# Kernel tuning notes

Measured on AMD Instinct MI355X. Metric: run time of the kernel, lower is better.

The kernel has to match this reference:

```python
import jax, jax.numpy as jnp
import numpy as np


def setup_inputs() -> dict:
    key = jax.random.key(0)
    k1, k2, k3 = jax.random.split(key, 3)
    vol_shape = (4, 1, 128, 192, 192)   # [B, C, D, H, W]
    dsc_shape = (4, 1, 8, 12, 12)       # PatchGAN-style discriminator logits
    return {
        "dsc_fake": jax.random.normal(k1, dsc_shape, dtype=jnp.float32),
        "predicts": jax.random.normal(k2, vol_shape, dtype=jnp.float32),
        "y_data": jax.random.normal(k3, vol_shape, dtype=jnp.float32),
        "zeros": jnp.zeros(dsc_shape, dtype=jnp.float32),
    }


def reference(dsc_fake, predicts, y_data, zeros):
    # BCE with logits (stable form), target = zeros
    bce = jnp.mean(
        jnp.maximum(dsc_fake, 0.0) - dsc_fake * zeros
        + jnp.log1p(jnp.exp(-jnp.abs(dsc_fake)))
    )
    # L1 loss between target volume and prediction
    g_loss_l1 = jnp.mean(jnp.abs(y_data - predicts))
    # Finite-difference gradient MSE along D, H, W (axes 2,3,4).
    # Original detaches to numpy, so this term carries no gradient.
    yd = jax.lax.stop_gradient(y_data)
    pr = jax.lax.stop_gradient(predicts)
    g_loss_gd = jnp.float32(0.0)
    for ax in (2, 3, 4):
        gy = jnp.abs(jnp.gradient(yd, axis=ax))   # central diff interior, one-sided edges
        gp = jnp.abs(jnp.gradient(pr, axis=ax))
        g_loss_gd = g_loss_gd + jnp.mean((gy - gp) ** 2)
    return bce + 100.0 * g_loss_l1 + 100.0 * g_loss_gd
```

## Files before the change

### kernel.cpp

```cpp
#include <hip/hip_runtime.h>
#include <math.h>

namespace {
constexpr int BATCH = 4;
constexpr int DDIM  = 128;
constexpr int HDIM  = 192;
constexpr int WDIM  = 192;
constexpr long long NTOT = (long long)BATCH * DDIM * HDIM * WDIM;
constexpr int GW    = WDIM / 4;
constexpr int NDSC  = 4 * 1 * 8 * 12 * 12;
constexpr int TH    = 8;
constexpr int SROWS = TH + 2;
constexpr int SGRP  = SROWS * GW;
constexpr int SFL   = SGRP * 4;
constexpr int BLOCK = 512;
constexpr int NWAVE = BLOCK / 64;
constexpr int NCHUNK = (SGRP + 63) / 64;
constexpr int NCOMP = TH * GW;
constexpr int DC    = 16;
constexpr int GRID  = BATCH * (HDIM / TH) * (DDIM / DC);
}

__device__ __forceinline__ float4 ld4(const float* __restrict__ p, long long g) {
    return *(const float4*)(p + 4LL * g);
}

__device__ __forceinline__ void stage2(const float* __restrict__ y,
                                       const float* __restrict__ p,
                                       long long fbase,
                                       float* ldsY, float* ldsP,
                                       int wave, int lane) {
    const int gbase = (wave == NCHUNK - 1) ? (SGRP - 64) : (wave * 64);
    __builtin_amdgcn_global_load_lds(
        (const __attribute__((address_space(1))) void*)(y + fbase + 4LL * (gbase + lane)),
        (__attribute__((address_space(3))) void*)(ldsY + 4 * gbase), 16, 0, 0);
    __builtin_amdgcn_global_load_lds(
        (const __attribute__((address_space(1))) void*)(p + fbase + 4LL * (gbase + lane)),
        (__attribute__((address_space(3))) void*)(ldsP + 4 * gbase), 16, 0, 0);
}

__global__ __launch_bounds__(BLOCK, 6) void vol_kernel(const float* __restrict__ p,
                                                       const float* __restrict__ y,
                                                       float* __restrict__ part) {
    __shared__ __align__(16) float smem[3][2][SFL];

    int bid = blockIdx.x;
    const int dIdx = bid % (DDIM / DC); bid /= (DDIM / DC);
    const int hIdx = bid % (HDIM / TH); bid /= (HDIM / TH);
    const int b    = bid;
    const int d0   = dIdx * DC;
    const int h0   = hIdx * TH;

    const int tid  = threadIdx.x;
    const int lane = tid & 63;
    const int wave = tid >> 6;
    const bool comp = (tid < NCOMP);

    const int g0 = (h0 == 0) ? 0 : ((h0 == HDIM - TH) ? (HDIM - SROWS) : (h0 - 1));
    const long long planeStride = (long long)HDIM * WDIM;
    const long long volBase = (long long)b * DDIM * planeStride + (long long)g0 * WDIM;

    stage2(y, p, volBase + (long long)d0 * planeStride,
           &smem[0][0][0], &smem[0][1][0], wave, lane);
    stage2(y, p, volBase + (long long)(d0 + 1) * planeStride,
           &smem[1][0][0], &smem[1][1][0], wave, lane);

    const int r  = tid / GW;
    const int gw = tid % GW;
    const int h  = h0 + r;
    const int rowOff = h0 - g0;
    const int sf  = ((r + rowOff) * GW + gw) * 4;
    const int hmF = ((h == 0)        ? 0 : -GW) * 4;
    const int hpF = ((h == HDIM - 1) ? 0 :  GW) * 4;
    const float sh  = (h == 0 || h == HDIM - 1) ? 1.f : 0.5f;
    const float swx = (gw == 0)      ? 1.f : 0.5f;
    const float sww = (gw == GW - 1) ? 1.f : 0.5f;
    const bool needL = (lane == 0)  && (gw > 0);
    const bool needR = (lane == 63) && (gw < GW - 1);

    float4 cm2y, cm1y, cm2p, cm1p;
    if (comp) {
        const int dm = (d0 > 0) ? (d0 - 1) : 0;
        const long long gown = (((long long)b * DDIM + dm) * HDIM + h) * GW + gw;
        cm1y = ld4(y, gown); cm1p = ld4(p, gown);
    }

    float l1 = 0.f, gd = 0.f;

    for (int i = 0; i <= DC; ++i) {
        if (i < DC) asm volatile("s_waitcnt vmcnt(2) lgkmcnt(0)" ::: "memory");
        else        asm volatile("s_waitcnt vmcnt(0) lgkmcnt(0)" ::: "memory");
        asm volatile("s_barrier" ::: "memory");

        if (i + 2 <= DC) {
            int dd = d0 + i + 2; if (dd > DDIM - 1) dd = DDIM - 1;
            const int s = (i + 2) % 3;
            stage2(y, p, volBase + (long long)dd * planeStride,
                   &smem[s][0][0], &smem[s][1][0], wave, lane);
        }

        if (comp) {
            const float* curY = &smem[i % 3][0][0];
            const float* curP = &smem[i % 3][1][0];
            const float4 c0y = *(const float4*)(curY + sf);
            const float4 c0p = *(const float4*)(curP + sf);

            if (i >= 1) {
                const int q = d0 + i - 1;
                const float sd = (q == 0 || q == DDIM - 1) ? 1.f : 0.5f;
                float t0;
                t0 = fabsf((c0y.x - cm2y.x) * sd) - fabsf((c0p.x - cm2p.x) * sd); gd += t0 * t0;
                t0 = fabsf((c0y.y - cm2y.y) * sd) - fabsf((c0p.y - cm2p.y) * sd); gd += t0 * t0;
                t0 = fabsf((c0y.z - cm2y.z) * sd) - fabsf((c0p.z - cm2p.z) * sd); gd += t0 * t0;
                t0 = fabsf((c0y.w - cm2y.w) * sd) - fabsf((c0p.w - cm2p.w) * sd); gd += t0 * t0;
            }

            if (i < DC) {
                l1 += fabsf(c0y.x - c0p.x) + fabsf(c0y.y - c0p.y)
                    + fabsf(c0y.z - c0p.z) + fabsf(c0y.w - c0p.w);

                float Ly = __shfl_up(c0y.w, 1, 64);
                float Lp = __shfl_up(c0p.w, 1, 64);
                float Ry = __shfl_down(c0y.x, 1, 64);
                float Rp = __shfl_down(c0p.x, 1, 64);
                if (needL) { Ly = curY[sf - 1]; Lp = curP[sf - 1]; }
                if (needR) { Ry = curY[sf + 4]; Rp = curP[sf + 4]; }
                Ly = gw ? Ly : c0y.x;             Lp = gw ? Lp : c0p.x;
                Ry = (gw == GW - 1) ? c0y.w : Ry; Rp = (gw == GW - 1) ? c0p.w : Rp;

                float t0, gy, gp;
                gy = (c0y.y - Ly) * swx;    gp = (c0p.y - Lp) * swx;
                t0 = fabsf(gy) - fabsf(gp); gd += t0 * t0;
                gy = (c0y.z - c0y.x) * 0.5f; gp = (c0p.z - c0p.x) * 0.5f;
                t0 = fabsf(gy) - fabsf(gp); gd += t0 * t0;
                gy = (c0y.w - c0y.y) * 0.5f; gp = (c0p.w - c0p.y) * 0.5f;
                t0 = fabsf(gy) - fabsf(gp); gd += t0 * t0;
                gy = (Ry - c0y.z) * sww;    gp = (Rp - c0p.z) * sww;
                t0 = fabsf(gy) - fabsf(gp); gd += t0 * t0;

                const float4 yhm = *(const float4*)(curY + sf + hmF);
                const float4 yhp = *(const float4*)(curY + sf + hpF);
                const float4 phm = *(const float4*)(curP + sf + hmF);
                const float4 php = *(const float4*)(curP + sf + hpF);
                t0 = fabsf((yhp.x - yhm.x) * sh) - fabsf((php.x - phm.x) * sh); gd += t0 * t0;
                t0 = fabsf((yhp.y - yhm.y) * sh) - fabsf((php.y - phm.y) * sh); gd += t0 * t0;
                t0 = fabsf((yhp.z - yhm.z) * sh) - fabsf((php.z - phm.z) * sh); gd += t0 * t0;
                t0 = fabsf((yhp.w - yhm.w) * sh) - fabsf((php.w - phm.w) * sh); gd += t0 * t0;
            }

            cm2y = cm1y; cm1y = c0y;
            cm2p = cm1p; cm1p = c0p;
        }
    }

    __shared__ float red1[NWAVE], red2[NWAVE];
    #pragma unroll
    for (int off = 32; off > 0; off >>= 1) {
        l1 += __shfl_down(l1, off, 64);
        gd += __shfl_down(gd, off, 64);
    }
    if (lane == 0) { red1[wave] = l1; red2[wave] = gd; }
    __syncthreads();
    if (tid == 0) {
        float s1 = 0.f, s2 = 0.f;
        #pragma unroll
        for (int w = 0; w < NWAVE; ++w) { s1 += red1[w]; s2 += red2[w]; }
        part[2 * blockIdx.x]     = s1;
        part[2 * blockIdx.x + 1] = s2;
    }
}

__global__ __launch_bounds__(256) void finalize_kernel(const float* __restrict__ dsc,
                                                       const float* __restrict__ part,
                                                       float* __restrict__ out) {
    float l1 = 0.f, gd = 0.f, s = 0.f;
    for (int i = threadIdx.x; i < GRID; i += 256) {
        l1 += part[2 * i];
        gd += part[2 * i + 1];
    }
    for (int i = threadIdx.x; i < NDSC; i += 256) {
        const float x = dsc[i];
        s += fmaxf(x, 0.f) + log1pf(expf(-fabsf(x)));
    }
    __shared__ float a[4], c[4], e[4];
    #pragma unroll
    for (int off = 32; off > 0; off >>= 1) {
        l1 += __shfl_down(l1, off, 64);
        gd += __shfl_down(gd, off, 64);
        s  += __shfl_down(s,  off, 64);
    }
    if ((threadIdx.x & 63) == 0) {
        const int w = threadIdx.x >> 6;
        a[w] = l1; c[w] = gd; e[w] = s;
    }
    __syncthreads();
    if (threadIdx.x == 0) {
        const float bce = (e[0] + e[1] + e[2] + e[3]) / (float)NDSC;
        const float l1m = (a[0] + a[1] + a[2] + a[3]) / (float)NTOT;
        const float gdm = (c[0] + c[1] + c[2] + c[3]) / (float)NTOT;
        out[0] = bce + 100.f * (l1m + gdm);
    }
}

extern "C" void kernel_launch(void* const* d_in, const int* in_sizes, int n_in,
                              void* d_out, int out_size, void* d_ws, size_t ws_size,
                              hipStream_t stream) {
    const float* dsc_fake = (const float*)d_in[0];
    const float* predicts = (const float*)d_in[1];
    const float* y_data   = (const float*)d_in[2];
    float* part = (float*)d_ws;
    float* out  = (float*)d_out;

    vol_kernel<<<GRID, BLOCK, 0, stream>>>(predicts, y_data, part);
    finalize_kernel<<<1, 256, 0, stream>>>(dsc_fake, part, out);
}
```

Before: 194.2 us.

## Fuse finalize into volume kernel with atomic ticket; enlarge tiles, double-buffer

Removes the separate finalize kernel. Each block now accumulates its partial sums with atomics, and the last block, found through a ticket counter, writes the final loss. The BCE term is spread across blocks. Tiles grow to 16 rows by 32 depth slices with 768-thread blocks, and the staging drops from three LDS buffers to two, using __syncthreads instead of hand-written waitcnt. This cuts launch overhead and halo re-reads but shortens the prefetch depth and lowers the block count, which may hurt latency hiding. It also adds a memset call and float atomic nondeterminism.

```diff
diff --git a/kernel.cpp b/kernel.cpp
--- a/kernel.cpp
+++ b/kernel.cpp
@@ -9,16 +9,16 @@
 constexpr long long NTOT = (long long)BATCH * DDIM * HDIM * WDIM;
 constexpr int GW    = WDIM / 4;
 constexpr int NDSC  = 4 * 1 * 8 * 12 * 12;
-constexpr int TH    = 8;
+constexpr int TH    = 16;
 constexpr int SROWS = TH + 2;
 constexpr int SGRP  = SROWS * GW;
 constexpr int SFL   = SGRP * 4;
-constexpr int BLOCK = 512;
+constexpr int BLOCK = TH * GW;
 constexpr int NWAVE = BLOCK / 64;
 constexpr int NCHUNK = (SGRP + 63) / 64;
-constexpr int NCOMP = TH * GW;
-constexpr int DC    = 16;
+constexpr int DC    = 32;
 constexpr int GRID  = BATCH * (HDIM / TH) * (DDIM / DC);
+constexpr int DSCPB = NDSC / GRID;
 }
 
 __device__ __forceinline__ float4 ld4(const float* __restrict__ p, long long g) {
@@ -30,19 +30,24 @@
                                        long long fbase,
                                        float* ldsY, float* ldsP,
                                        int wave, int lane) {
-    const int gbase = (wave == NCHUNK - 1) ? (SGRP - 64) : (wave * 64);
-    __builtin_amdgcn_global_load_lds(
-        (const __attribute__((address_space(1))) void*)(y + fbase + 4LL * (gbase + lane)),
-        (__attribute__((address_space(3))) void*)(ldsY + 4 * gbase), 16, 0, 0);
-    __builtin_amdgcn_global_load_lds(
-        (const __attribute__((address_space(1))) void*)(p + fbase + 4LL * (gbase + lane)),
-        (__attribute__((address_space(3))) void*)(ldsP + 4 * gbase), 16, 0, 0);
+    for (int c = wave; c < NCHUNK; c += NWAVE) {
+        const int gbase = (c == NCHUNK - 1) ? (SGRP - 64) : (c * 64);
+        __builtin_amdgcn_global_load_lds(
+            (const __attribute__((address_space(1))) void*)(y + fbase + 4LL * (gbase + lane)),
+            (__attribute__((address_space(3))) void*)(ldsY + 4 * gbase), 16, 0, 0);
+        __builtin_amdgcn_global_load_lds(
+            (const __attribute__((address_space(1))) void*)(p + fbase + 4LL * (gbase + lane)),
+            (__attribute__((address_space(3))) void*)(ldsP + 4 * gbase), 16, 0, 0);
+    }
 }
 
-__global__ __launch_bounds__(BLOCK, 6) void vol_kernel(const float* __restrict__ p,
-                                                       const float* __restrict__ y,
-                                                       float* __restrict__ part) {
-    __shared__ __align__(16) float smem[3][2][SFL];
+__global__ __launch_bounds__(BLOCK) void vol_kernel(const float* __restrict__ p,
+                                                    const float* __restrict__ y,
+                                                    const float* __restrict__ dsc,
+                                                    float* __restrict__ acc,
+                                                    int* __restrict__ ticket,
+                                                    float* __restrict__ out) {
+    __shared__ __align__(16) float smem[2][2][SFL];
 
     int bid = blockIdx.x;
     const int dIdx = bid % (DDIM / DC); bid /= (DDIM / DC);
@@ -54,7 +59,6 @@
     const int tid  = threadIdx.x;
     const int lane = tid & 63;
     const int wave = tid >> 6;
-    const bool comp = (tid < NCOMP);
 
     const int g0 = (h0 == 0) ? 0 : ((h0 == HDIM - TH) ? (HDIM - SROWS) : (h0 - 1));
     const long long planeStride = (long long)HDIM * WDIM;
@@ -62,8 +66,6 @@
 
     stage2(y, p, volBase + (long long)d0 * planeStride,
            &smem[0][0][0], &smem[0][1][0], wave, lane);
-    stage2(y, p, volBase + (long long)(d0 + 1) * planeStride,
-           &smem[1][0][0], &smem[1][1][0], wave, lane);
 
     const int r  = tid / GW;
     const int gw = tid % GW;
@@ -78,127 +80,105 @@
     const bool needL = (lane == 0)  && (gw > 0);
     const bool needR = (lane == 63) && (gw < GW - 1);
 
-    float4 cm2y, cm1y, cm2p, cm1p;
-    if (comp) {
-        const int dm = (d0 > 0) ? (d0 - 1) : 0;
-        const long long gown = (((long long)b * DDIM + dm) * HDIM + h) * GW + gw;
-        cm1y = ld4(y, gown); cm1p = ld4(p, gown);
+    const int dm = (d0 > 0) ? (d0 - 1) : 0;
+    const long long gown = (((long long)b * DDIM + dm) * HDIM + h) * GW + gw;
+    float4 cm1y = ld4(y, gown), cm1p = ld4(p, gown);
+    float4 cm2y, cm2p;
+
+    float bc = 0.f;
+    if (tid < DSCPB) {
+        const float x = dsc[blockIdx.x * DSCPB + tid];
+        bc = fmaxf(x, 0.f) + log1pf(expf(-fabsf(x)));
     }
 
     float l1 = 0.f, gd = 0.f;
 
     for (int i = 0; i <= DC; ++i) {
-        if (i < DC) asm volatile("s_waitcnt vmcnt(2) lgkmcnt(0)" ::: "memory");
-        else        asm volatile("s_waitcnt vmcnt(0) lgkmcnt(0)" ::: "memory");
-        asm volatile("s_barrier" ::: "memory");
+        __syncthreads();
 
-        if (i + 2 <= DC) {
-            int dd = d0 + i + 2; if (dd > DDIM - 1) dd = DDIM - 1;
-            const int s = (i + 2) % 3;
+        if (i < DC) {
+            int dd = d0 + i + 1; if (dd > DDIM - 1) dd = DDIM - 1;
+            const int s = (i + 1) & 1;
             stage2(y, p, volBase + (long long)dd * planeStride,
                    &smem[s][0][0], &smem[s][1][0], wave, lane);
         }
 
-        if (comp) {
-            const float* curY = &smem[i % 3][0][0];
-            const float* curP = &smem[i % 3][1][0];
-            const float4 c0y = *(const float4*)(curY + sf);
-            const float4 c0p = *(const float4*)(curP + sf);
+        const float* curY = &smem[i & 1][0][0];
+        const float* curP = &smem[i & 1][1][0];
+        const float4 c0y = *(const float4*)(curY + sf);
+        const float4 c0p = *(const float4*)(curP + sf);
 
-            if (i >= 1) {
-                const int q = d0 + i - 1;
-                const float sd = (q == 0 || q == DDIM - 1) ? 1.f : 0.5f;
-                float t0;
-                t0 = fabsf((c0y.x - cm2y.x) * sd) - fabsf((c0p.x - cm2p.x) * sd); gd += t0 * t0;
-                t0 = fabsf((c0y.y - cm2y.y) * sd) - fabsf((c0p.y - cm2p.y) * sd); gd += t0 * t0;
-                t0 = fabsf((c0y.z - cm2y.z) * sd) - fabsf((c0p.z - cm2p.z) * sd); gd += t0 * t0;
-                t0 = fabsf((c0y.w - cm2y.w) * sd) - fabsf((c0p.w - cm2p.w) * sd); gd += t0 * t0;
-            }
+        if (i >= 1) {
+            const int q = d0 + i - 1;
+            const float sd = (q == 0 || q == DDIM - 1) ? 1.f : 0.5f;
+            float t0;
+            t0 = fabsf((c0y.x - cm2y.x) * sd) - fabsf((c0p.x - cm2p.x) * sd); gd += t0 * t0;
+            t0 = fabsf((c0y.y - cm2y.y) * sd) - fabsf((c0p.y - cm2p.y) * sd); gd += t0 * t0;
+            t0 = fabsf((c0y.z - cm2y.z) * sd) - fabsf((c0p.z - cm2p.z) * sd); gd += t0 * t0;
+            t0 = fabsf((c0y.w - cm2y.w) * sd) - fabsf((c0p.w - cm2p.w) * sd); gd += t0 * t0;
+        }
 
-            if (i < DC) {
-                l1 += fabsf(c0y.x - c0p.x) + fabsf(c0y.y - c0p.y)
-                    + fabsf(c0y.z - c0p.z) + fabsf(c0y.w - c0p.w);
+        if (i < DC) {
+            l1 += fabsf(c0y.x - c0p.x) + fabsf(c0y.y - c0p.y)
+                + fabsf(c0y.z - c0p.z) + fabsf(c0y.w - c0p.w);
 
-                float Ly = __shfl_up(c0y.w, 1, 64);
-                float Lp = __shfl_up(c0p.w, 1, 64);
-                float Ry = __shfl_down(c0y.x, 1, 64);
-                float Rp = __shfl_down(c0p.x, 1, 64);
-                if (needL) { Ly = curY[sf - 1]; Lp = curP[sf - 1]; }
-                if (needR) { Ry = curY[sf + 4]; Rp = curP[sf + 4]; }
-                Ly = gw ? Ly : c0y.x;             Lp = gw ? Lp : c0p.x;
-                Ry = (gw == GW - 1) ? c0y.w : Ry; Rp = (gw == GW - 1) ? c0p.w : Rp;
+            float Ly = __shfl_up(c0y.w, 1, 64);
+            float Lp = __shfl_up(c0p.w, 1, 64);
+            float Ry = __shfl_down(c0y.x, 1, 64);
+            float Rp = __shfl_down(c0p.x, 1, 64);
+            if (needL) { Ly = curY[sf - 1]; Lp = curP[sf - 1]; }
+            if (needR) { Ry = curY[sf + 4]; Rp = curP[sf + 4]; }
+            Ly = gw ? Ly : c0y.x;             Lp = gw ? Lp : c0p.x;
+            Ry = (gw == GW - 1) ? c0y.w : Ry; Rp = (gw == GW - 1) ? c0p.w : Rp;
 
-                float t0, gy, gp;
-                gy = (c0y.y - Ly) * swx;    gp = (c0p.y - Lp) * swx;
-                t0 = fabsf(gy) - fabsf(gp); gd += t0 * t0;
-                gy = (c0y.z - c0y.x) * 0.5f; gp = (c0p.z - c0p.x) * 0.5f;
-                t0 = fabsf(gy) - fabsf(gp); gd += t0 * t0;
-                gy = (c0y.w - c0y.y) * 0.5f; gp = (c0p.w - c0p.y) * 0.5f;
-                t0 = fabsf(gy) - fabsf(gp); gd += t0 * t0;
-                gy = (Ry - c0y.z) * sww;    gp = (Rp - c0p.z) * sww;
-                t0 = fabsf(gy) - fabsf(gp); gd += t0 * t0;
+            float t0, gy, gp;
+            gy = (c0y.y - Ly) * swx;     gp = (c0p.y - Lp) * swx;
+            t0 = fabsf(gy) - fabsf(gp);  gd += t0 * t0;
+            gy = (c0y.z - c0y.x) * 0.5f; gp = (c0p.z - c0p.x) * 0.5f;
+            t0 = fabsf(gy) - fabsf(gp);  gd += t0 * t0;
+            gy = (c0y.w - c0y.y) * 0.5f; gp = (c0p.w - c0p.y) * 0.5f;
+            t0 = fabsf(gy) - fabsf(gp);  gd += t0 * t0;
+            gy = (Ry - c0y.z) * sww;     gp = (Rp - c0p.z) * sww;
+            t0 = fabsf(gy) - fabsf(gp);  gd += t0 * t0;
 
-                const float4 yhm = *(const float4*)(curY + sf + hmF);
-                const float4 yhp = *(const float4*)(curY + sf + hpF);
-                const float4 phm = *(const float4*)(curP + sf + hmF);
-                const float4 php = *(const float4*)(curP + sf + hpF);
-                t0 = fabsf((yhp.x - yhm.x) * sh) - fabsf((php.x - phm.x) * sh); gd += t0 * t0;
-                t0 = fabsf((yhp.y - yhm.y) * sh) - fabsf((php.y - phm.y) * sh); gd += t0 * t0;
-                t0 = fabsf((yhp.z - yhm.z) * sh) - fabsf((php.z - phm.z) * sh); gd += t0 * t0;
-                t0 = fabsf((yhp.w - yhm.w) * sh) - fabsf((php.w - phm.w) * sh); gd += t0 * t0;
-            }
+            const float4 yhm = *(const float4*)(curY + sf + hmF);
+            const float4 yhp = *(const float4*)(curY + sf + hpF);
+            const float4 phm = *(const float4*)(curP + sf + hmF);
+            const float4 php = *(const float4*)(curP + sf + hpF);
+            t0 = fabsf((yhp.x - yhm.x) * sh) - fabsf((php.x - phm.x) * sh); gd += t0 * t0;
+            t0 = fabsf((yhp.y - yhm.y) * sh) - fabsf((php.y - phm.y) * sh); gd += t0 * t0;
+            t0 = fabsf((yhp.z - yhm.z) * sh) - fabsf((php.z - phm.z) * sh); gd += t0 * t0;
+            t0 = fabsf((yhp.w - yhm.w) * sh) - fabsf((php.w - phm.w) * sh); gd += t0 * t0;
+        }
 
-            cm2y = cm1y; cm1y = c0y;
-            cm2p = cm1p; cm1p = c0p;
-        }
+        cm2y = cm1y; cm1y = c0y;
+        cm2p = cm1p; cm1p = c0p;
     }
 
-    __shared__ float red1[NWAVE], red2[NWAVE];
+    __shared__ float r1[NWAVE], r2[NWAVE], r3[NWAVE];
     #pragma unroll
     for (int off = 32; off > 0; off >>= 1) {
         l1 += __shfl_down(l1, off, 64);
         gd += __shfl_down(gd, off, 64);
+        bc += __shfl_down(bc, off, 64);
     }
-    if (lane == 0) { red1[wave] = l1; red2[wave] = gd; }
+    if (lane == 0) { r1[wave] = l1; r2[wave] = gd; r3[wave] = bc; }
     __syncthreads();
     if (tid == 0) {
-        float s1 = 0.f, s2 = 0.f;
+        float s1 = 0.f, s2 = 0.f, s3 = 0.f;
         #pragma unroll
-        for (int w = 0; w < NWAVE; ++w) { s1 += red1[w]; s2 += red2[w]; }
-        part[2 * blockIdx.x]     = s1;
-        part[2 * blockIdx.x + 1] = s2;
-    }
-}
-
-__global__ __launch_bounds__(256) void finalize_kernel(const float* __restrict__ dsc,
-                                                       const float* __restrict__ part,
-                                                       float* __restrict__ out) {
-    float l1 = 0.f, gd = 0.f, s = 0.f;
-    for (int i = threadIdx.x; i < GRID; i += 256) {
-        l1 += part[2 * i];
-        gd += part[2 * i + 1];
-    }
-    for (int i = threadIdx.x; i < NDSC; i += 256) {
-        const float x = dsc[i];
-        s += fmaxf(x, 0.f) + log1pf(expf(-fabsf(x)));
-    }
-    __shared__ float a[4], c[4], e[4];
-    #pragma unroll
-    for (int off = 32; off > 0; off >>= 1) {
-        l1 += __shfl_down(l1, off, 64);
-        gd += __shfl_down(gd, off, 64);
-        s  += __shfl_down(s,  off, 64);
-    }
-    if ((threadIdx.x & 63) == 0) {
-        const int w = threadIdx.x >> 6;
-        a[w] = l1; c[w] = gd; e[w] = s;
-    }
-    __syncthreads();
-    if (threadIdx.x == 0) {
-        const float bce = (e[0] + e[1] + e[2] + e[3]) / (float)NDSC;
-        const float l1m = (a[0] + a[1] + a[2] + a[3]) / (float)NTOT;
-        const float gdm = (c[0] + c[1] + c[2] + c[3]) / (float)NTOT;
-        out[0] = bce + 100.f * (l1m + gdm);
+        for (int w = 0; w < NWAVE; ++w) { s1 += r1[w]; s2 += r2[w]; s3 += r3[w]; }
+        atomicAdd(&acc[0], s1);
+        atomicAdd(&acc[1], s2);
+        atomicAdd(&acc[2], s3);
+        __threadfence();
+        const int t = atomicAdd(ticket, 1);
+        if (t == GRID - 1) {
+            const float L = atomicAdd(&acc[0], 0.f);
+            const float G = atomicAdd(&acc[1], 0.f);
+            const float B = atomicAdd(&acc[2], 0.f);
+            out[0] = B / (float)NDSC + 100.f * ((L + G) / (float)NTOT);
+        }
     }
 }
 
@@ -208,9 +188,10 @@
     const float* dsc_fake = (const float*)d_in[0];
     const float* predicts = (const float*)d_in[1];
     const float* y_data   = (const float*)d_in[2];
-    float* part = (float*)d_ws;
-    float* out  = (float*)d_out;
+    float* acc    = (float*)d_ws;
+    int*   ticket = (int*)((char*)d_ws + 3 * sizeof(float));
+    float* out    = (float*)d_out;
 
-    vol_kernel<<<GRID, BLOCK, 0, stream>>>(predicts, y_data, part);
-    finalize_kernel<<<1, 256, 0, stream>>>(dsc_fake, part, out);
+    hipMemsetAsync(d_ws, 0, 4 * sizeof(float), stream);
+    vol_kernel<<<GRID, BLOCK, 0, stream>>>(predicts, y_data, dsc_fake, acc, ticket, out);
 }
```

New measurement: 193.2 us. No clear change (-0.5%).
